# Performance work log

Measured on AMD Instinct MI355X. Metric: run time of the kernel, lower is better.

The kernel has to match this reference:

```python
import jax, jax.numpy as jnp
import numpy as np

N = 20000          # nodes
E = 320000         # edges
C = 64             # channel multiplicity (64x0e node feats)
NATTR = 10         # node attr (species one-hot) dim
EDGE_FEAT = 8      # radial bessel features
L_DIMS = (1, 3, 5) # irrep dims for l = 0,1,2
RAD = [64, 64, 64]
AVG_NEIGH = 16.0
NUM_L = len(L_DIMS)


def setup_inputs() -> dict:
    key = jax.random.key(0)
    ks = jax.random.split(key, 12)
    node_attrs = jax.random.uniform(ks[0], (N, NATTR), dtype=jnp.float32)
    node_feats = jax.random.normal(ks[1], (N, C), dtype=jnp.float32)
    edge_attrs = jax.random.normal(ks[2], (E, sum(L_DIMS)), dtype=jnp.float32)
    edge_feats = jax.random.normal(ks[3], (E, EDGE_FEAT), dtype=jnp.float32)
    edge_index = jax.random.randint(ks[4], (2, E), 0, N, dtype=jnp.int64)
    # linear1: o3.Linear(64x0e -> 64x0e)
    W_lin1 = jax.random.normal(ks[5], (C, C), dtype=jnp.float32)
    # radial MLP: FullyConnectedNet([8,64,64,64,192], Identity)
    W_r0 = jax.random.normal(ks[6], (EDGE_FEAT, RAD[0]), dtype=jnp.float32)
    W_r1 = jax.random.normal(ks[7], (RAD[0], RAD[1]), dtype=jnp.float32)
    W_r2 = jax.random.normal(ks[8], (RAD[1], RAD[2]), dtype=jnp.float32)
    W_r3 = jax.random.normal(ks[9], (RAD[2], NUM_L * C), dtype=jnp.float32)
    # post-aggregation linear: o3.Linear(64x0e+64x1o+64x2e -> same), per-l 64x64 mix
    W_msg = jax.random.normal(ks[10], (NUM_L, C, C), dtype=jnp.float32)
    # skip_tp: FullyConnectedTensorProduct(64x0e, 10x0e -> 64x0e), 'uvw'
    W_skip = jax.random.normal(ks[11], (C, NATTR, C), dtype=jnp.float32)
    return {
        "node_attrs": node_attrs, "node_feats": node_feats,
        "edge_attrs": edge_attrs, "edge_feats": edge_feats,
        "edge_index": edge_index,
        "W_lin1": W_lin1, "W_r0": W_r0, "W_r1": W_r1, "W_r2": W_r2,
        "W_r3": W_r3, "W_msg": W_msg, "W_skip": W_skip,
    }


def reference(node_attrs, node_feats, edge_attrs, edge_feats, edge_index,
              W_lin1, W_r0, W_r1, W_r2, W_r3, W_msg, W_skip):
    sender, receiver = edge_index[0], edge_index[1]
    num_nodes = node_feats.shape[0]
    num_edges = edge_feats.shape[0]

    # linear1 (o3.Linear on scalars): fan_in normalized
    h = node_feats @ (W_lin1 / np.float32(np.sqrt(C)))           # [N, C]

    # radial MLP (e3nn FullyConnectedNet, identity activation)
    w = edge_feats
    for W in (W_r0, W_r1, W_r2, W_r3):
        w = w @ (W / np.float32(np.sqrt(W.shape[0])))
    tp_w = w.reshape(num_edges, NUM_L, C)                        # per-l 'uvu' weights

    # edge gather + weighted tensor product (0e x l -> l per channel)
    xs = h[sender]                                               # [E, C]
    blocks = []
    off = 0
    for l, d in enumerate(L_DIMS):
        y_l = edge_attrs[:, off:off + d]                         # [E, d]
        m_l = (xs * tp_w[:, l, :])[:, :, None] * y_l[:, None, :] # [E, C, d]
        blocks.append(m_l.reshape(num_edges, C * d))
        off += d
    mji = jnp.concatenate(blocks, axis=-1)                       # [E, C*9]

    # scatter-sum to receivers
    msg = jax.ops.segment_sum(mji, receiver, num_segments=num_nodes)  # [N, C*9]

    # per-l linear mix + avg-neighbor norm, then reshape_irreps -> [N, C, 9]
    out_blocks = []
    off = 0
    for l, d in enumerate(L_DIMS):
        m_l = msg[:, off:off + C * d].reshape(num_nodes, C, d)
        o_l = jnp.einsum('num,uv->nvm', m_l, W_msg[l]) / np.float32(np.sqrt(C))
        out_blocks.append(o_l)
        off += C * d
    out = jnp.concatenate(out_blocks, axis=-1) / np.float32(AVG_NEIGH)  # [N, C, 9]

    # self connection: FullyConnectedTensorProduct(64x0e, 10x0e -> 64x0e)
    sc = jnp.einsum('nu,nv,uvw->nw', h, node_attrs, W_skip) / np.float32(np.sqrt(C * NATTR))
    return out, sc
```

## Files before the change

kernel.cpp:

```cpp
#include <hip/hip_runtime.h>

#define N_NODES 20000
#define N_EDGES 320000
#define C 64
#define NATTR 10
#define MSG_DIM 576
#define WC_COLS 192
#define PRE 12
#define REC 20

__global__ __launch_bounds__(256) void node_linear_hist(
        const float* __restrict__ nf,
        const float* __restrict__ W,
        float* __restrict__ h,
        const int* __restrict__ eidx,
        int* __restrict__ counts) {
    const int t = threadIdx.x;
    {
        const int e = blockIdx.x * 256 + t;
        atomicAdd(&counts[eidx[N_EDGES + e]], 1);
    }
    __shared__ float Ws[64 * 64];
    __shared__ float row[4][64];
    const int lane = t & 63, wv = t >> 6;
    for (int i = t; i < 4096; i += 256) Ws[i] = W[i] * 0.125f;
    __syncthreads();
    const int base = blockIdx.x * 16;
    #pragma unroll 1
    for (int it = 0; it < 4; ++it) {
        const int n = base + it * 4 + wv;
        row[wv][lane] = nf[(size_t)n * 64 + lane];
        float acc = 0.f;
        #pragma unroll
        for (int k = 0; k < 64; ++k) acc += row[wv][k] * Ws[k * 64 + lane];
        h[(size_t)n * 64 + lane] = acc;
    }
}

#define SCAN_PER 20
__global__ __launch_bounds__(1024) void scan_radial_kernel(
        const int* __restrict__ counts,
        int* __restrict__ start, int* __restrict__ cursor,
        const float* __restrict__ Wr0, const float* __restrict__ Wr1,
        const float* __restrict__ Wr2, const float* __restrict__ Wr3,
        float* __restrict__ Wc, float* __restrict__ rec) {
    __shared__ int wsum[16];
    __shared__ float T[8 * 64];
    __shared__ float T2[8 * 64];
    const int t = threadIdx.x, lane = t & 63, w = t >> 6;
    const float s0r = 0.35355339059327373f;
    const float s1r = 0.125f;

    const int base = t * SCAN_PER;
    int v[SCAN_PER];
    int s = 0;
    #pragma unroll
    for (int j = 0; j < SCAN_PER; ++j) {
        const int idx = base + j;
        v[j] = (idx < N_NODES) ? counts[idx] : 0;
        s += v[j];
    }
    int sc = s;
    #pragma unroll
    for (int off = 1; off < 64; off <<= 1) {
        int up = __shfl_up(sc, off);
        if (lane >= off) sc += up;
    }
    if (lane == 63) wsum[w] = sc;
    if (t < 16) rec[(size_t)(N_EDGES + t) * REC + 17] = 0.f;
    for (int i = t; i < 8 * 64; i += 1024) {
        int r = i >> 6, c2 = i & 63;
        float acc = 0.f;
        for (int k = 0; k < 64; ++k) acc += Wr0[r * 64 + k] * Wr1[k * 64 + c2];
        T[i] = acc * (s0r * s1r);
    }
    __syncthreads();
    if (t == 0) {
        int a = 0;
        #pragma unroll
        for (int i = 0; i < 16; ++i) { int x = wsum[i]; wsum[i] = a; a += x; }
    }
    for (int i = t; i < 8 * 64; i += 1024) {
        int r = i >> 6, c2 = i & 63;
        float acc = 0.f;
        for (int k = 0; k < 64; ++k) acc += T[r * 64 + k] * Wr2[k * 64 + c2];
        T2[i] = acc * s1r;
    }
    __syncthreads();
    int a = wsum[w] + (sc - s);
    #pragma unroll
    for (int j = 0; j < SCAN_PER; ++j) {
        const int idx = base + j;
        if (idx < N_NODES) {
            start[idx] = a;
            cursor[idx] = a;
            a += v[j];
        }
    }
    for (int i = t; i < 8 * WC_COLS; i += 1024) {
        int r = i / WC_COLS, c2 = i % WC_COLS;
        float acc = 0.f;
        for (int k = 0; k < 64; ++k) acc += T2[r * 64 + k] * Wr3[k * WC_COLS + c2];
        Wc[i] = acc * s1r;
    }
}

__global__ __launch_bounds__(256) void scatter_skip(
        const int* __restrict__ eidx,
        const float* __restrict__ ef,
        const float* __restrict__ ea,
        int* __restrict__ cursor,
        float* __restrict__ rec,
        const float* __restrict__ h,
        const float* __restrict__ attrs,
        const float* __restrict__ Wskip,
        float* __restrict__ sc) {
    __shared__ __align__(16) float hl[32 * 64];
    __shared__ __align__(16) float wch[5120];
    const int t = threadIdx.x;

    if (blockIdx.x < 1250) {
        const int e = blockIdx.x * 256 + t;
        const int r = eidx[N_EDGES + e];
        const int s = eidx[e];
        const int pos = atomicAdd(&cursor[r], 1);
        const float4* f4 = reinterpret_cast<const float4*>(ef + (size_t)e * 8);
        const float* y = ea + (size_t)e * 9;
        float4* o = reinterpret_cast<float4*>(rec + (size_t)pos * REC);
        o[0] = f4[0];
        o[1] = f4[1];
        o[2] = make_float4(y[0], y[1], y[2], y[3]);
        o[3] = make_float4(y[4], y[5], y[6], y[7]);
        o[4] = make_float4(y[8], __int_as_float(s), 0.f, 0.f);
        return;
    }

    const int lane = t & 63, wv = t >> 6;
    const int base = (blockIdx.x - 1250) * 32;
    {
        const float4* src = reinterpret_cast<const float4*>(h + (size_t)base * 64);
        float4* dst = reinterpret_cast<float4*>(hl);
        #pragma unroll
        for (int i = 0; i < 2; ++i) dst[t + 256 * i] = src[t + 256 * i];
    }
    float alr[8][NATTR];
    #pragma unroll
    for (int i = 0; i < 8; ++i) {
        const float* ap = attrs + (size_t)(base + wv + 4 * i) * NATTR;
        #pragma unroll
        for (int v = 0; v < NATTR; ++v) alr[i][v] = ap[v];
    }
    float acc[8] = {0.f, 0.f, 0.f, 0.f, 0.f, 0.f, 0.f, 0.f};
    __syncthreads();

    #pragma unroll 1
    for (int ch = 0; ch < 8; ++ch) {
        {
            const float4* src = reinterpret_cast<const float4*>(Wskip + ch * 5120);
            float4* dst = reinterpret_cast<float4*>(wch);
            #pragma unroll
            for (int i = 0; i < 5; ++i) dst[t + 256 * i] = src[t + 256 * i];
        }
        __syncthreads();
        #pragma unroll 1
        for (int uu = 0; uu < 8; ++uu) {
            const int u = ch * 8 + uu;
            float tmp[8] = {0.f, 0.f, 0.f, 0.f, 0.f, 0.f, 0.f, 0.f};
            #pragma unroll
            for (int v = 0; v < NATTR; ++v) {
                const float wk = wch[(uu * NATTR + v) * 64 + lane];
                #pragma unroll
                for (int i = 0; i < 8; ++i) tmp[i] += alr[i][v] * wk;
            }
            #pragma unroll
            for (int i = 0; i < 8; ++i)
                acc[i] += hl[(wv + 4 * i) * 64 + u] * tmp[i];
        }
        __syncthreads();
    }
    const float scale = 0.03952847075210474f;
    #pragma unroll
    for (int i = 0; i < 8; ++i)
        sc[(size_t)(base + wv + 4 * i) * 64 + lane] = acc[i] * scale;
}

__global__ __launch_bounds__(256) void gather_fused(
                              const float* __restrict__ rec,
                              const float* __restrict__ h,
                              const float* __restrict__ Wc,
                              const float* __restrict__ Wmsg,
                              const int* __restrict__ start,
                              const int* __restrict__ counts,
                              float* __restrict__ out) {
    __shared__ float part[2][9][64];
    __shared__ __align__(16) float erec[4][PRE * REC];
    const int t = threadIdx.x, lane = t & 63, wv = t >> 6;
    const int g = wv >> 1;
    const int half = wv & 1;
    const int n = blockIdx.x * 2 + g;

    float wc0[8], wc1[8], wc2[8];
    #pragma unroll
    for (int k = 0; k < 8; ++k) {
        wc0[k] = Wc[k * WC_COLS + lane];
        wc1[k] = Wc[k * WC_COLS + 64 + lane];
        wc2[k] = Wc[k * WC_COLS + 128 + lane];
    }

    const int s0 = start[n], cnt = counts[n];
    const int jbeg = half ? (cnt >> 1) : 0;
    const int jend = half ? cnt : (cnt >> 1);
    const int m = jend - jbeg;
    const int base = s0 + jbeg;

    if (lane < PRE * REC / 4) {
        const float4 v = *reinterpret_cast<const float4*>(
            rec + (size_t)base * REC + lane * 4);
        *reinterpret_cast<float4*>(&erec[wv][lane * 4]) = v;
    }
    __syncthreads();

    float p0 = 0.f;
    float p1[3] = {0.f, 0.f, 0.f};
    float p2[5] = {0.f, 0.f, 0.f, 0.f, 0.f};

    const int P = (m < PRE) ? m : PRE;
    int snd[PRE];
    #pragma unroll
    for (int b = 0; b < PRE; ++b) snd[b] = __float_as_int(erec[wv][b * REC + 17]);
    float xs[PRE];
    #pragma unroll
    for (int b = 0; b < PRE; ++b) {
        const int sb = (b < P) ? snd[b] : snd[0];
        xs[b] = h[(size_t)sb * 64 + lane];
    }

    #pragma unroll
    for (int j = 0; j < PRE; ++j) {
        if (j < P) {
            const float* er = &erec[wv][j * REC];
            const float4 e0 = *reinterpret_cast<const float4*>(er);
            const float4 e1 = *reinterpret_cast<const float4*>(er + 4);
            const float4 ya = *reinterpret_cast<const float4*>(er + 8);
            const float4 yb = *reinterpret_cast<const float4*>(er + 12);
            const float  y8 = er[16];
            const float* fk = reinterpret_cast<const float*>(&e0);
            const float* gk = reinterpret_cast<const float*>(&e1);
            float w0 = fk[0] * wc0[0], w1 = fk[0] * wc1[0], w2 = fk[0] * wc2[0];
            #pragma unroll
            for (int k = 1; k < 4; ++k) {
                w0 += fk[k] * wc0[k]; w1 += fk[k] * wc1[k]; w2 += fk[k] * wc2[k];
            }
            #pragma unroll
            for (int k = 0; k < 4; ++k) {
                w0 += gk[k] * wc0[k + 4]; w1 += gk[k] * wc1[k + 4]; w2 += gk[k] * wc2[k + 4];
            }
            const float b0 = xs[j] * w0, b1 = xs[j] * w1, b2 = xs[j] * w2;
            p0    += b0 * ya.x;
            p1[0] += b1 * ya.y; p1[1] += b1 * ya.z; p1[2] += b1 * ya.w;
            p2[0] += b2 * yb.x; p2[1] += b2 * yb.y; p2[2] += b2 * yb.z;
            p2[3] += b2 * yb.w; p2[4] += b2 * y8;
        }
    }
    for (int j = PRE; j < m; ++j) {
        const float4* q = reinterpret_cast<const float4*>(rec + (size_t)(base + j) * REC);
        const float4 fa = q[0], fb = q[1];
        const float4 ya = q[2], yb = q[3], yc = q[4];
        const int snd_t = __float_as_int(yc.y);
        const float xs_t = h[(size_t)snd_t * 64 + lane];
        const float* fk = reinterpret_cast<const float*>(&fa);
        const float* gk = reinterpret_cast<const float*>(&fb);
        float w0 = fk[0] * wc0[0], w1 = fk[0] * wc1[0], w2 = fk[0] * wc2[0];
        #pragma unroll
        for (int k = 1; k < 4; ++k) {
            w0 += fk[k] * wc0[k]; w1 += fk[k] * wc1[k]; w2 += fk[k] * wc2[k];
        }
        #pragma unroll
        for (int k = 0; k < 4; ++k) {
            w0 += gk[k] * wc0[k + 4]; w1 += gk[k] * wc1[k + 4]; w2 += gk[k] * wc2[k + 4];
        }
        const float b0 = xs_t * w0, b1 = xs_t * w1, b2 = xs_t * w2;
        p0    += b0 * ya.x;
        p1[0] += b1 * ya.y; p1[1] += b1 * ya.z; p1[2] += b1 * ya.w;
        p2[0] += b2 * yb.x; p2[1] += b2 * yb.y; p2[2] += b2 * yb.z;
        p2[3] += b2 * yb.w; p2[4] += b2 * yc.x;
    }

    if (half) {
        part[g][0][lane] = p0;
        #pragma unroll
        for (int m2 = 0; m2 < 3; ++m2) part[g][1 + m2][lane] = p1[m2];
        #pragma unroll
        for (int m2 = 0; m2 < 5; ++m2) part[g][4 + m2][lane] = p2[m2];
    }
    __syncthreads();
    if (!half) {
        part[g][0][lane] += p0;
        #pragma unroll
        for (int m2 = 0; m2 < 3; ++m2) part[g][1 + m2][lane] += p1[m2];
        #pragma unroll
        for (int m2 = 0; m2 < 5; ++m2) part[g][4 + m2][lane] += p2[m2];
    }
    __syncthreads();

    const float scale = 1.f / 128.f;
    float* op = out + (size_t)n * MSG_DIM + lane * 9;
    if (!half) {
        float o0 = 0.f, o1 = 0.f, o2 = 0.f, o3 = 0.f;
        #pragma unroll 8
        for (int u = 0; u < 64; ++u) {
            const float wv0 = Wmsg[u * 64 + lane];
            const float wv1 = Wmsg[4096 + u * 64 + lane];
            o0 += part[g][0][u] * wv0;
            o1 += part[g][1][u] * wv1;
            o2 += part[g][2][u] * wv1;
            o3 += part[g][3][u] * wv1;
        }
        op[0] = o0 * scale;
        op[1] = o1 * scale;
        op[2] = o2 * scale;
        op[3] = o3 * scale;
    } else {
        float o4 = 0.f, o5 = 0.f, o6 = 0.f, o7 = 0.f, o8 = 0.f;
        #pragma unroll 8
        for (int u = 0; u < 64; ++u) {
            const float wv2 = Wmsg[8192 + u * 64 + lane];
            o4 += part[g][4][u] * wv2;
            o5 += part[g][5][u] * wv2;
            o6 += part[g][6][u] * wv2;
            o7 += part[g][7][u] * wv2;
            o8 += part[g][8][u] * wv2;
        }
        op[4] = o4 * scale;
        op[5] = o5 * scale;
        op[6] = o6 * scale;
        op[7] = o7 * scale;
        op[8] = o8 * scale;
    }
}

extern "C" void kernel_launch(void* const* d_in, const int* in_sizes, int n_in,
                              void* d_out, int out_size, void* d_ws, size_t ws_size,
                              hipStream_t stream) {
    const float* node_attrs = (const float*)d_in[0];
    const float* node_feats = (const float*)d_in[1];
    const float* edge_attrs = (const float*)d_in[2];
    const float* edge_feats = (const float*)d_in[3];
    const int*   edge_index = (const int*)d_in[4];
    const float* W_lin1 = (const float*)d_in[5];
    const float* W_r0 = (const float*)d_in[6];
    const float* W_r1 = (const float*)d_in[7];
    const float* W_r2 = (const float*)d_in[8];
    const float* W_r3 = (const float*)d_in[9];
    const float* W_msg = (const float*)d_in[10];
    const float* W_skip = (const float*)d_in[11];

    float* out = (float*)d_out;
    float* sc  = out + (size_t)N_NODES * MSG_DIM;

    float* wsf = (float*)d_ws;
    float* Wc = wsf;
    float* h  = wsf + 2048;
    int* wsi   = (int*)(wsf + 2048 + (size_t)N_NODES * 64);
    int* counts = wsi;
    int* start  = wsi + N_NODES;
    int* cursor = wsi + 2 * N_NODES;
    float* rec  = (float*)(wsi + 3 * N_NODES);

    hipMemsetAsync(counts, 0, N_NODES * sizeof(int), stream);
    node_linear_hist<<<1250, 256, 0, stream>>>(node_feats, W_lin1, h,
                                               edge_index, counts);
    scan_radial_kernel<<<1, 1024, 0, stream>>>(counts, start, cursor,
                                               W_r0, W_r1, W_r2, W_r3, Wc, rec);
    scatter_skip<<<1875, 256, 0, stream>>>(
        edge_index, edge_feats, edge_attrs, cursor, rec,
        h, node_attrs, W_skip, sc);
    gather_fused<<<N_NODES / 2, 256, 0, stream>>>(
        rec, h, Wc, W_msg, start, counts, out);
}
```

Measured before the change: 214.4 us.

## Rebalance kernel fusion: node linear into scatter, skip TP into gather

Moves the node linear (h = nf·W_lin1) out of the histogram kernel and into the scatter kernel as extra blocks. Moves the skip tensor-product blocks from the scatter kernel into the gather kernel as extra leading blocks. The skip path now reads W_skip directly from global/L1 rather than staging it through shared memory in chunks. Shared memory in the gather kernel is unioned into one buffer. The aim is to shorten the serial histogram and scan stages and overlap the skip compute with the gather. The cost is skip blocks running ahead of gather blocks and uncached-in-LDS weight reads.

```diff
diff --git a/kernel.cpp b/kernel.cpp
--- a/kernel.cpp
+++ b/kernel.cpp
@@ -9,32 +9,9 @@
 #define PRE 12
 #define REC 20
 
-__global__ __launch_bounds__(256) void node_linear_hist(
-        const float* __restrict__ nf,
-        const float* __restrict__ W,
-        float* __restrict__ h,
-        const int* __restrict__ eidx,
-        int* __restrict__ counts) {
-    const int t = threadIdx.x;
-    {
-        const int e = blockIdx.x * 256 + t;
-        atomicAdd(&counts[eidx[N_EDGES + e]], 1);
-    }
-    __shared__ float Ws[64 * 64];
-    __shared__ float row[4][64];
-    const int lane = t & 63, wv = t >> 6;
-    for (int i = t; i < 4096; i += 256) Ws[i] = W[i] * 0.125f;
-    __syncthreads();
-    const int base = blockIdx.x * 16;
-    #pragma unroll 1
-    for (int it = 0; it < 4; ++it) {
-        const int n = base + it * 4 + wv;
-        row[wv][lane] = nf[(size_t)n * 64 + lane];
-        float acc = 0.f;
-        #pragma unroll
-        for (int k = 0; k < 64; ++k) acc += row[wv][k] * Ws[k * 64 + lane];
-        h[(size_t)n * 64 + lane] = acc;
-    }
+__global__ void hist_kernel(const int* __restrict__ eidx, int* __restrict__ counts) {
+    const int e = blockIdx.x * 256 + threadIdx.x;
+    atomicAdd(&counts[eidx[N_EDGES + e]], 1);
 }
 
 #define SCAN_PER 20
@@ -105,18 +82,17 @@
     }
 }
 
-__global__ __launch_bounds__(256) void scatter_skip(
+__global__ __launch_bounds__(256) void scatter_nl(
         const int* __restrict__ eidx,
         const float* __restrict__ ef,
         const float* __restrict__ ea,
         int* __restrict__ cursor,
         float* __restrict__ rec,
-        const float* __restrict__ h,
-        const float* __restrict__ attrs,
-        const float* __restrict__ Wskip,
-        float* __restrict__ sc) {
-    __shared__ __align__(16) float hl[32 * 64];
-    __shared__ __align__(16) float wch[5120];
+        const float* __restrict__ nf,
+        const float* __restrict__ W,
+        float* __restrict__ h) {
+    __shared__ float Ws[64 * 64];
+    __shared__ float row[4][64];
     const int t = threadIdx.x;
 
     if (blockIdx.x < 1250) {
@@ -136,68 +112,77 @@
     }
 
     const int lane = t & 63, wv = t >> 6;
-    const int base = (blockIdx.x - 1250) * 32;
-    {
-        const float4* src = reinterpret_cast<const float4*>(h + (size_t)base * 64);
-        float4* dst = reinterpret_cast<float4*>(hl);
-        #pragma unroll
-        for (int i = 0; i < 2; ++i) dst[t + 256 * i] = src[t + 256 * i];
-    }
-    float alr[8][NATTR];
-    #pragma unroll
-    for (int i = 0; i < 8; ++i) {
-        const float* ap = attrs + (size_t)(base + wv + 4 * i) * NATTR;
-        #pragma unroll
-        for (int v = 0; v < NATTR; ++v) alr[i][v] = ap[v];
-    }
-    float acc[8] = {0.f, 0.f, 0.f, 0.f, 0.f, 0.f, 0.f, 0.f};
-    __syncthreads();
-
+    for (int i = t; i < 4096; i += 256) Ws[i] = W[i] * 0.125f;
+    __syncthreads();
+    const int base = (blockIdx.x - 1250) * 16;
     #pragma unroll 1
-    for (int ch = 0; ch < 8; ++ch) {
-        {
-            const float4* src = reinterpret_cast<const float4*>(Wskip + ch * 5120);
-            float4* dst = reinterpret_cast<float4*>(wch);
-            #pragma unroll
-            for (int i = 0; i < 5; ++i) dst[t + 256 * i] = src[t + 256 * i];
-        }
-        __syncthreads();
-        #pragma unroll 1
-        for (int uu = 0; uu < 8; ++uu) {
-            const int u = ch * 8 + uu;
-            float tmp[8] = {0.f, 0.f, 0.f, 0.f, 0.f, 0.f, 0.f, 0.f};
-            #pragma unroll
-            for (int v = 0; v < NATTR; ++v) {
-                const float wk = wch[(uu * NATTR + v) * 64 + lane];
-                #pragma unroll
-                for (int i = 0; i < 8; ++i) tmp[i] += alr[i][v] * wk;
-            }
-            #pragma unroll
-            for (int i = 0; i < 8; ++i)
-                acc[i] += hl[(wv + 4 * i) * 64 + u] * tmp[i];
-        }
-        __syncthreads();
-    }
-    const float scale = 0.03952847075210474f;
-    #pragma unroll
-    for (int i = 0; i < 8; ++i)
-        sc[(size_t)(base + wv + 4 * i) * 64 + lane] = acc[i] * scale;
-}
-
-__global__ __launch_bounds__(256) void gather_fused(
+    for (int it = 0; it < 4; ++it) {
+        const int n = base + it * 4 + wv;
+        row[wv][lane] = nf[(size_t)n * 64 + lane];
+        float acc = 0.f;
+        #pragma unroll
+        for (int k = 0; k < 64; ++k) acc += row[wv][k] * Ws[k * 64 + lane];
+        h[(size_t)n * 64 + lane] = acc;
+    }
+}
+
+__global__ __launch_bounds__(256) void gather_skip(
                               const float* __restrict__ rec,
                               const float* __restrict__ h,
                               const float* __restrict__ Wc,
                               const float* __restrict__ Wmsg,
                               const int* __restrict__ start,
                               const int* __restrict__ counts,
-                              float* __restrict__ out) {
-    __shared__ float part[2][9][64];
-    __shared__ __align__(16) float erec[4][PRE * REC];
+                              float* __restrict__ out,
+                              const float* __restrict__ attrs,
+                              const float* __restrict__ Wskip,
+                              float* __restrict__ sc) {
+    __shared__ __align__(16) float smem[2112];
     const int t = threadIdx.x, lane = t & 63, wv = t >> 6;
+
+    if (blockIdx.x < 625) {
+        float* hl = smem;
+        const int base = blockIdx.x * 32;
+        {
+            const float4* src = reinterpret_cast<const float4*>(h + (size_t)base * 64);
+            float4* dst = reinterpret_cast<float4*>(hl);
+            dst[t] = src[t];
+            dst[t + 256] = src[t + 256];
+        }
+        float alr[8][NATTR];
+        #pragma unroll
+        for (int i = 0; i < 8; ++i) {
+            const float* ap = attrs + (size_t)(base + wv + 4 * i) * NATTR;
+            #pragma unroll
+            for (int v = 0; v < NATTR; ++v) alr[i][v] = ap[v];
+        }
+        float acc[8] = {0.f, 0.f, 0.f, 0.f, 0.f, 0.f, 0.f, 0.f};
+        __syncthreads();
+        #pragma unroll 1
+        for (int u = 0; u < 64; ++u) {
+            float tmp[8] = {0.f, 0.f, 0.f, 0.f, 0.f, 0.f, 0.f, 0.f};
+            #pragma unroll
+            for (int v = 0; v < NATTR; ++v) {
+                const float wk = Wskip[(u * NATTR + v) * 64 + lane];
+                #pragma unroll
+                for (int i = 0; i < 8; ++i) tmp[i] += alr[i][v] * wk;
+            }
+            #pragma unroll
+            for (int i = 0; i < 8; ++i)
+                acc[i] += hl[(wv + 4 * i) * 64 + u] * tmp[i];
+        }
+        const float scale = 0.03952847075210474f;
+        #pragma unroll
+        for (int i = 0; i < 8; ++i)
+            sc[(size_t)(base + wv + 4 * i) * 64 + lane] = acc[i] * scale;
+        return;
+    }
+
+    float (*part)[9][64] = reinterpret_cast<float(*)[9][64]>(smem);
+    float (*erec)[PRE * REC] = reinterpret_cast<float(*)[PRE * REC]>(smem + 1152);
     const int g = wv >> 1;
     const int half = wv & 1;
-    const int n = blockIdx.x * 2 + g;
+    const int n = (blockIdx.x - 625) * 2 + g;
 
     float wc0[8], wc1[8], wc2[8];
     #pragma unroll
@@ -368,13 +353,13 @@
     float* rec  = (float*)(wsi + 3 * N_NODES);
 
     hipMemsetAsync(counts, 0, N_NODES * sizeof(int), stream);
-    node_linear_hist<<<1250, 256, 0, stream>>>(node_feats, W_lin1, h,
-                                               edge_index, counts);
+    hist_kernel<<<1250, 256, 0, stream>>>(edge_index, counts);
     scan_radial_kernel<<<1, 1024, 0, stream>>>(counts, start, cursor,
                                                W_r0, W_r1, W_r2, W_r3, Wc, rec);
-    scatter_skip<<<1875, 256, 0, stream>>>(
+    scatter_nl<<<2500, 256, 0, stream>>>(
         edge_index, edge_feats, edge_attrs, cursor, rec,
-        h, node_attrs, W_skip, sc);
-    gather_fused<<<N_NODES / 2, 256, 0, stream>>>(
-        rec, h, Wc, W_msg, start, counts, out);
-}
+        node_feats, W_lin1, h);
+    gather_skip<<<10625, 256, 0, stream>>>(
+        rec, h, Wc, W_msg, start, counts, out,
+        node_attrs, W_skip, sc);
+}
```

New measurement: 203.4 us, median of 3. 5.1% less time.
